# Optimization experiments

Measured on AMD Instinct MI355X. Metric: run time of the kernel, lower is better.

The kernel has to match this reference:

```python
import jax, jax.numpy as jnp
import numpy as np

GRID_MIN = np.array([-40.0, -40.0, -2.0], dtype=np.float32)
VOXEL = 0.8
NZ, NY, NX = 10, 100, 100
NVOX = NZ * NY * NX


def setup_inputs() -> dict:
    key = jax.random.key(0)
    ks = jax.random.split(key, 7)
    B, T, V, H, W = 1, 2, 6, 32, 88
    Cg, Co = 48, 256
    lo = jnp.asarray(GRID_MIN)
    hi = jnp.array([40.0, 40.0, 6.0], dtype=jnp.float32)
    u = jax.random.uniform(ks[0], (B, T, V, H, W, 3), dtype=jnp.float32)
    centers = lo + u * (hi - lo)
    gs_features = jax.random.normal(ks[1], (B, T, V, H, W, Cg), dtype=jnp.float32)
    occ_volume = jax.random.normal(ks[2], (B, T, Co, NZ, NY, NX), dtype=jnp.float32)
    W_g2o = jax.random.normal(ks[3], (Cg, Co), dtype=jnp.float32) * 0.1
    b_g2o = jnp.zeros((Co,), dtype=jnp.float32)
    W_o2g = jax.random.normal(ks[4], (Co, Cg), dtype=jnp.float32) * 0.1
    b_o2g = jnp.zeros((Cg,), dtype=jnp.float32)
    return {"centers": centers, "gs_features": gs_features, "occ_volume": occ_volume,
            "W_g2o": W_g2o, "b_g2o": b_g2o, "W_o2g": W_o2g, "b_o2g": b_o2g}


def _scatter_mean(pts, vals):
    # pts: [BT, N, 3], vals: [BT, N, C] -> dense [BT, NVOX, C] voxel means
    BT, N, C = vals.shape
    mins = jnp.asarray(GRID_MIN, dtype=pts.dtype)
    ijk = jnp.floor((pts - mins) / VOXEL).astype(jnp.int32)
    ix, iy, iz = ijk[..., 0], ijk[..., 1], ijk[..., 2]
    valid = (ix >= 0) & (ix < NX) & (iy >= 0) & (iy < NY) & (iz >= 0) & (iz < NZ)
    lin = (jnp.clip(iz, 0, NZ - 1) * (NY * NX)
           + jnp.clip(iy, 0, NY - 1) * NX
           + jnp.clip(ix, 0, NX - 1))
    seg = (jnp.arange(BT, dtype=jnp.int32)[:, None] * NVOX + lin).reshape(-1)
    m = valid.reshape(-1, 1).astype(vals.dtype)
    vsum = jax.ops.segment_sum(vals.reshape(-1, C) * m, seg, num_segments=BT * NVOX)
    cnt = jax.ops.segment_sum(m, seg, num_segments=BT * NVOX)
    return (vsum / jnp.maximum(cnt, 1.0)).reshape(BT, NVOX, C)


def _trilinear_sample(occ_sp, pts):
    # occ_sp: [BT, NVOX, C] (z-major), pts: [BT, N, 3] metric xyz
    # grid_sample semantics: align_corners=False, padding_mode='zeros'
    mins = jnp.asarray(GRID_MIN, dtype=pts.dtype)
    dims = jnp.array([NX * VOXEL, NY * VOXEL, NZ * VOXEL], dtype=pts.dtype)
    g = (pts - mins) / jnp.maximum(dims, 1e-6) * 2.0 - 1.0  # normalized xyz in [-1,1]
    sizes = jnp.array([NX, NY, NZ], dtype=pts.dtype)
    pix = ((g + 1.0) * sizes - 1.0) * 0.5  # unnormalized pixel coords (x,y,z)
    p0 = jnp.floor(pix)
    frac = pix - p0  # fractional part, weight of the +1 corner
    p0i = p0.astype(jnp.int32)
    out = jnp.zeros(occ_sp.shape[:1] + pts.shape[1:2] + occ_sp.shape[-1:], occ_sp.dtype)
    bounds = (NX, NY, NZ)
    for dz in (0, 1):
        for dy in (0, 1):
            for dx in (0, 1):
                d = (dx, dy, dz)
                idxs = [p0i[..., a] + d[a] for a in range(3)]
                inb = ((idxs[0] >= 0) & (idxs[0] < NX)
                       & (idxs[1] >= 0) & (idxs[1] < NY)
                       & (idxs[2] >= 0) & (idxs[2] < NZ))
                w = jnp.ones_like(frac[..., 0])
                for a in range(3):
                    w = w * jnp.where(d[a] == 1, frac[..., a], 1.0 - frac[..., a])
                lin = (jnp.clip(idxs[2], 0, NZ - 1) * (NY * NX)
                       + jnp.clip(idxs[1], 0, NY - 1) * NX
                       + jnp.clip(idxs[0], 0, NX - 1))
                corner = jnp.take_along_axis(occ_sp, lin[..., None], axis=1)
                out = out + corner * (w * inb.astype(w.dtype))[..., None]
    return out  # [BT, N, C]


def reference(centers, gs_features, occ_volume, W_g2o, b_g2o, W_o2g, b_o2g):
    B, T, V, H, W, _ = centers.shape
    BT, N = B * T, V * H * W
    Co = occ_volume.shape[2]
    pts = centers.reshape(BT, N, 3)
    feats = gs_features.reshape(BT, N, gs_features.shape[-1])
    # gs -> occ: linear proj then voxel scatter-mean
    vals = feats @ W_g2o + b_g2o  # [BT, N, Co]
    vol = _scatter_mean(pts, vals)  # [BT, NVOX, Co]
    gs_to_occ = vol.reshape(B, T, NZ, NY, NX, Co).transpose(0, 1, 5, 2, 3, 4)
    # occ -> gs: trilinear sample then linear proj
    occ_sp = occ_volume.reshape(BT, Co, NVOX).transpose(0, 2, 1)  # [BT, NVOX, Co]
    sampled = _trilinear_sample(occ_sp, pts)  # [BT, N, Co]
    occ_to_gs = (sampled @ W_o2g + b_o2g).reshape(B, T, V, H, W, -1)
    return gs_to_occ, occ_to_gs
```

## Files before the change

kernel.cpp:

```cpp
#include <hip/hip_runtime.h>
#include <hip/hip_bf16.h>

typedef float v4f __attribute__((ext_vector_type(4)));
typedef short v4s __attribute__((ext_vector_type(4)));
typedef short bfrag8 __attribute__((ext_vector_type(8)));

constexpr int NXc = 100, NYc = 100, NZc = 10;
constexpr int NVOX = NZc * NYc * NXc;
constexpr int CO = 256, CG = 48;
constexpr int BT = 2;
constexpr int NPT = 6 * 32 * 88;
constexpr int NPTS = BT * NPT;
constexpr int MAXS = NPTS;
constexpr int NW64 = (NVOX + 63) / 64;
constexpr int NB_VP = (BT * NW64 + 3) / 4;
constexpr int NB_SC = NPTS * CG / 256;
constexpr int NB_WV = (NVOX + 1023) / 1024;
constexpr int NB_WR = NB_WV * 8 * BT;
constexpr int NB_GA = NPTS * CG / 256;
constexpr float GMX = -40.0f, GMY = -40.0f, GMZ = -2.0f;
constexpr float VOXEL = 0.8f;

static __device__ __forceinline__ short f2bf(float f) {
    __hip_bfloat16 h = __float2bfloat16(f);
    return __builtin_bit_cast(short, h);
}
static __device__ __forceinline__ float bf2f(unsigned short u) {
    unsigned v = (unsigned)u << 16;
    return __builtin_bit_cast(float, v);
}

__global__ __launch_bounds__(256) void k_init(
    v4f* __restrict__ p, int n16,
    const float* __restrict__ Wo2g, short* __restrict__ wp)
{
    if (blockIdx.x < 1024) {
        v4f z = {0.f, 0.f, 0.f, 0.f};
        for (int i = blockIdx.x * 256 + threadIdx.x; i < n16; i += 1024 * 256)
            p[i] = z;
    } else {
        for (int e = threadIdx.x; e < 8 * 3 * 64 * 8; e += 256) {
            int j  = e & 7;
            int l  = (e >> 3) & 63;
            int ft = e >> 9;
            int s  = ft / 3, gt = ft - 3 * s;
            int k  = s * 32 + (l >> 4) * 8 + j;
            int g  = gt * 16 + (l & 15);
            wp[e] = f2bf(Wo2g[k * CG + g]);
        }
    }
}

__global__ __launch_bounds__(256) void k_count(
    const float* __restrict__ pts, float* __restrict__ cnt,
    int* __restrict__ nocc, int* __restrict__ invmap, int* __restrict__ ptvox,
    int* __restrict__ list)
{
    int pn = blockIdx.x * 256 + threadIdx.x;
    float x = pts[pn * 3 + 0];
    float y = pts[pn * 3 + 1];
    float z = pts[pn * 3 + 2];
    int ix = (int)floorf((x - GMX) / VOXEL);
    int iy = (int)floorf((y - GMY) / VOXEL);
    int iz = (int)floorf((z - GMZ) / VOXEL);
    bool valid = (ix >= 0 && ix < NXc && iy >= 0 && iy < NYc && iz >= 0 && iz < NZc);
    if (!valid) { ptvox[pn] = -1; return; }
    int bt = pn / NPT;
    int btvox = bt * NVOX + iz * (NYc * NXc) + iy * NXc + ix;
    ptvox[pn] = btvox;
    float old = atomicAdd(&cnt[btvox], 1.0f);
    if (old == 0.0f) {
        int s = atomicAdd(nocc, 1);
        invmap[btvox] = s + 1;
        list[s] = btvox;
    }
}

__global__ __launch_bounds__(256) void k_megaA(
    const float* __restrict__ occ, const short* __restrict__ wp,
    unsigned short* __restrict__ P,
    const float* __restrict__ feats, const int* __restrict__ ptvox,
    const int* __restrict__ invmap, float* __restrict__ compactM)
{
    int bid = blockIdx.x;
    int vpq = bid / 9;
    bool is_vp = (bid % 9 == 0) && (vpq < NB_VP);
    if (is_vp) {
        int gwid = (vpq * 256 + threadIdx.x) >> 6;
        if (gwid >= BT * NW64) return;
        int l = threadIdx.x & 63;
        int q = l >> 4, r = l & 15;
        const bfrag8* wf = reinterpret_cast<const bfrag8*>(wp);
        bfrag8 wfr[8][3];
#pragma unroll
        for (int s = 0; s < 8; ++s)
#pragma unroll
            for (int gt = 0; gt < 3; ++gt)
                wfr[s][gt] = wf[(s * 3 + gt) * 64 + l];
        int bt = gwid / NW64;
        int vox0 = (gwid - bt * NW64) * 64;
        int vbase = vox0 + 4 * r;
        int vload = vbase > NVOX - 4 ? NVOX - 4 : vbase;
        const float* b0 = occ + (size_t)bt * CO * NVOX + (size_t)q * 8 * NVOX + vload;
        v4f acc[4][3];
#pragma unroll
        for (int t = 0; t < 4; ++t)
#pragma unroll
            for (int gt = 0; gt < 3; ++gt)
                acc[t][gt] = v4f{0.f, 0.f, 0.f, 0.f};
#pragma unroll
        for (int s = 0; s < 8; ++s) {
            v4f vj[8];
#pragma unroll
            for (int j = 0; j < 8; ++j)
                vj[j] = *reinterpret_cast<const v4f*>(b0 + (size_t)(s * 32 + j) * NVOX);
            bfrag8 bf[4];
#pragma unroll
            for (int t = 0; t < 4; ++t)
#pragma unroll
                for (int j = 0; j < 8; ++j)
                    bf[t][j] = f2bf(vj[j][t]);
#pragma unroll
            for (int t = 0; t < 4; ++t)
#pragma unroll
                for (int gt = 0; gt < 3; ++gt)
                    acc[t][gt] = __builtin_amdgcn_mfma_f32_16x16x32_bf16(
                        wfr[s][gt], bf[t], acc[t][gt], 0, 0, 0);
        }
        unsigned short* o = P + ((size_t)bt * NVOX + vbase) * CG + q * 4;
#pragma unroll
        for (int t = 0; t < 4; ++t) {
            if (vbase + t < NVOX) {
#pragma unroll
                for (int gt = 0; gt < 3; ++gt) {
                    v4s pk;
#pragma unroll
                    for (int e = 0; e < 4; ++e) pk[e] = f2bf(acc[t][gt][e]);
                    *reinterpret_cast<v4s*>(o + t * CG + gt * 16) = pk;
                }
            }
        }
    } else {
        int nvp = (bid + 8) / 9; if (nvp > NB_VP) nvp = NB_VP;
        int scid = bid - nvp;
        int idx = scid * 256 + threadIdx.x;
        int k  = idx % CG;
        int pn = idx / CG;
        int bv = ptvox[pn];
        if (bv < 0) return;
        int slot = invmap[bv] - 1;
        atomicAdd(&compactM[(size_t)slot * CG + k], feats[idx]);
    }
}

__global__ __launch_bounds__(256) void k_gemm(
    const float* __restrict__ compactM, const float* __restrict__ cnt,
    const int* __restrict__ list, const int* __restrict__ noccp,
    const float* __restrict__ Wg2o, const float* __restrict__ bg2o,
    float* __restrict__ compact256)
{
    int nocc = *noccp;
    int s0 = blockIdx.x * 32;
    if (s0 >= nocc) return;
    __shared__ float Wl[CG * CO];
    __shared__ float Ml[32 * CG];
    for (int j = threadIdx.x; j < CG * CO; j += 256) Wl[j] = Wg2o[j];
    for (int j = threadIdx.x; j < 32 * CG; j += 256) {
        int v = j / CG, k = j - v * CG;
        int slot = s0 + v;
        float m = 0.f;
        if (slot < nocc) {
            int btvox = list[slot];
            m = compactM[(size_t)slot * CG + k] / cnt[btvox];
        }
        Ml[j] = m;
    }
    __syncthreads();
    int wid = threadIdx.x >> 6, l = threadIdx.x & 63;
    int vb = wid * 8;
    float4 bias = *reinterpret_cast<const float4*>(&bg2o[4 * l]);
    float acc[8][4];
#pragma unroll
    for (int v = 0; v < 8; ++v) {
        acc[v][0] = bias.x; acc[v][1] = bias.y; acc[v][2] = bias.z; acc[v][3] = bias.w;
    }
    for (int k = 0; k < CG; k += 4) {
        float4 w0 = *reinterpret_cast<const float4*>(&Wl[(k + 0) * CO + 4 * l]);
        float4 w1 = *reinterpret_cast<const float4*>(&Wl[(k + 1) * CO + 4 * l]);
        float4 w2 = *reinterpret_cast<const float4*>(&Wl[(k + 2) * CO + 4 * l]);
        float4 w3 = *reinterpret_cast<const float4*>(&Wl[(k + 3) * CO + 4 * l]);
#pragma unroll
        for (int v = 0; v < 8; ++v) {
            float4 m4 = *reinterpret_cast<const float4*>(&Ml[(vb + v) * CG + k]);
            acc[v][0] = fmaf(m4.x, w0.x, acc[v][0]);
            acc[v][1] = fmaf(m4.x, w0.y, acc[v][1]);
            acc[v][2] = fmaf(m4.x, w0.z, acc[v][2]);
            acc[v][3] = fmaf(m4.x, w0.w, acc[v][3]);
            acc[v][0] = fmaf(m4.y, w1.x, acc[v][0]);
            acc[v][1] = fmaf(m4.y, w1.y, acc[v][1]);
            acc[v][2] = fmaf(m4.y, w1.z, acc[v][2]);
            acc[v][3] = fmaf(m4.y, w1.w, acc[v][3]);
            acc[v][0] = fmaf(m4.z, w2.x, acc[v][0]);
            acc[v][1] = fmaf(m4.z, w2.y, acc[v][1]);
            acc[v][2] = fmaf(m4.z, w2.z, acc[v][2]);
            acc[v][3] = fmaf(m4.z, w2.w, acc[v][3]);
            acc[v][0] = fmaf(m4.w, w3.x, acc[v][0]);
            acc[v][1] = fmaf(m4.w, w3.y, acc[v][1]);
            acc[v][2] = fmaf(m4.w, w3.z, acc[v][2]);
            acc[v][3] = fmaf(m4.w, w3.w, acc[v][3]);
        }
    }
#pragma unroll
    for (int v = 0; v < 8; ++v) {
        int slot = s0 + vb + v;
        if (slot < nocc) {
            float4 rr; rr.x = acc[v][0]; rr.y = acc[v][1]; rr.z = acc[v][2]; rr.w = acc[v][3];
            *reinterpret_cast<float4*>(&compact256[(size_t)slot * CO + 4 * l]) = rr;
        }
    }
}

__global__ __launch_bounds__(256) void k_megaB(
    const int* __restrict__ invmap, const float* __restrict__ compact256,
    float* __restrict__ out0,
    const float* __restrict__ pts, const unsigned short* __restrict__ P,
    const float* __restrict__ bo2g, float* __restrict__ out1)
{
    __shared__ float ldsT[32][260];
    int bid = blockIdx.x;
    int wrq = bid / 5;
    bool is_wr = (bid % 5 == 0) && (wrq < NB_WR);
    if (is_wr) {
        int bt  = wrq / (NB_WV * 8);
        int rem = wrq - bt * (NB_WV * 8);
        int c0  = (rem / NB_WV) * 32;
        int vb  = (rem - (rem / NB_WV) * NB_WV) * 1024;
        int tid = threadIdx.x;
        int w = tid >> 6, l = tid & 63;
        float* ob = out0 + (size_t)bt * CO * NVOX;
#pragma unroll
        for (int sc = 0; sc < 4; ++sc) {
            int vbase = vb + sc * 256;
            int vox = vbase + tid;
            int slot = (vox < NVOX) ? invmap[bt * NVOX + vox] : 0;
            if (slot > 0) {
                const v4f* row = reinterpret_cast<const v4f*>(
                    compact256 + (size_t)(slot - 1) * CO + c0);
#pragma unroll
                for (int cq = 0; cq < 8; ++cq) {
                    v4f d = row[cq];
#pragma unroll
                    for (int i = 0; i < 4; ++i) ldsT[cq * 4 + i][tid] = d[i];
                }
            } else {
#pragma unroll
                for (int c = 0; c < 32; ++c) ldsT[c][tid] = 0.f;
            }
            __syncthreads();
#pragma unroll
            for (int u = 0; u < 8; ++u) {
                int ci = u * 4 + w;
                int vq = 4 * l;
                int vv = vbase + vq;
                if (vv < NVOX) {
                    v4f val = *reinterpret_cast<const v4f*>(&ldsT[ci][vq]);
                    __builtin_nontemporal_store(val,
                        reinterpret_cast<v4f*>(ob + (size_t)(c0 + ci) * NVOX + vv));
                }
            }
            if (sc < 3) __syncthreads();
        }
    } else {
        int nwr = (bid + 4) / 5; if (nwr > NB_WR) nwr = NB_WR;
        int gaid = bid - nwr;
        int idx = gaid * 256 + threadIdx.x;
        int g  = idx % CG;
        int pn = idx / CG;
        int bt = pn / NPT;
        float x = pts[pn * 3 + 0];
        float y = pts[pn * 3 + 1];
        float z = pts[pn * 3 + 2];
        float gx = (x - GMX) / 80.0f * 2.0f - 1.0f;
        float gy = (y - GMY) / 80.0f * 2.0f - 1.0f;
        float gz = (z - GMZ) / 8.0f  * 2.0f - 1.0f;
        float px = ((gx + 1.0f) * (float)NXc - 1.0f) * 0.5f;
        float py = ((gy + 1.0f) * (float)NYc - 1.0f) * 0.5f;
        float pz = ((gz + 1.0f) * (float)NZc - 1.0f) * 0.5f;
        float fx = floorf(px), fy = floorf(py), fz = floorf(pz);
        float rx = px - fx, ry = py - fy, rz = pz - fz;
        int x0 = (int)fx, y0 = (int)fy, z0 = (int)fz;
        float acc = bo2g[g];
        const unsigned short* Pb = P + (size_t)bt * NVOX * CG;
#pragma unroll
        for (int dz = 0; dz <= 1; ++dz) {
            int zi = z0 + dz;
            if (zi < 0 || zi >= NZc) continue;
            float wz = dz ? rz : 1.0f - rz;
#pragma unroll
            for (int dy = 0; dy <= 1; ++dy) {
                int yi = y0 + dy;
                if (yi < 0 || yi >= NYc) continue;
                float wy = dy ? ry : 1.0f - ry;
#pragma unroll
                for (int dx = 0; dx <= 1; ++dx) {
                    int xi = x0 + dx;
                    if (xi < 0 || xi >= NXc) continue;
                    float wx = dx ? rx : 1.0f - rx;
                    float w = (wx * wy) * wz;
                    int lin = zi * (NYc * NXc) + yi * NXc + xi;
                    acc = fmaf(w, bf2f(Pb[(size_t)lin * CG + g]), acc);
                }
            }
        }
        out1[idx] = acc;
    }
}

extern "C" void kernel_launch(void* const* d_in, const int* in_sizes, int n_in,
                              void* d_out, int out_size, void* d_ws, size_t ws_size,
                              hipStream_t stream)
{
    const float* centers = (const float*)d_in[0];
    const float* feats   = (const float*)d_in[1];
    const float* occ     = (const float*)d_in[2];
    const float* Wg2o    = (const float*)d_in[3];
    const float* bg2o    = (const float*)d_in[4];
    const float* Wo2g    = (const float*)d_in[5];
    const float* bo2g    = (const float*)d_in[6];

    float* out  = (float*)d_out;
    float* out0 = out;
    float* out1 = out + (size_t)BT * CO * NVOX;
    short* wp   = (short*)out1;

    char* w = (char*)d_ws;
    float* cnt       = (float*)w;                 w += (size_t)BT * NVOX * 4;
    int*   nocc      = (int*)w;                   w += 256;
    int*   invmap    = (int*)w;                   w += (size_t)BT * NVOX * 4;
    float* compactM  = (float*)w;                 w += (size_t)MAXS * CG * 4;
    size_t zbytes = (size_t)BT * NVOX * 4 + 256 + (size_t)BT * NVOX * 4
                  + (size_t)MAXS * CG * 4;
    int*   ptvox     = (int*)w;                   w += (size_t)NPTS * 4;
    int*   list      = (int*)w;                   w += (size_t)MAXS * 4;
    float* compact256= (float*)w;                 w += (size_t)MAXS * CO * 4;
    unsigned short* P = (unsigned short*)w;

    k_init<<<1025, 256, 0, stream>>>((v4f*)d_ws, (int)(zbytes / 16), Wo2g, wp);
    k_count<<<NPTS / 256, 256, 0, stream>>>(centers, cnt, nocc, invmap, ptvox, list);
    k_megaA<<<NB_VP + NB_SC, 256, 0, stream>>>(occ, wp, P, feats, ptvox, invmap, compactM);
    k_gemm<<<(MAXS + 31) / 32, 256, 0, stream>>>(compactM, cnt, list, nocc, Wg2o, bg2o, compact256);
    k_megaB<<<NB_WR + NB_GA, 256, 0, stream>>>(invmap, compact256, out0, centers, P, bo2g, out1);
}
```

Before: 144.9 us.

## Store compact voxel means as bf16 and stream weight fragments in megaA

The compacted per-voxel 256-channel projection buffer is now written in bf16 by the gemm kernel and converted back to float when megaB transposes it into the dense output. This halves intermediate traffic for the gather-transpose stage. megaA also stops preloading all 24 weight fragments into registers, loading each per step instead, and adds a launch-bounds occupancy hint to cut register pressure. The cost is bf16 rounding in the gs_to_occ output and extra weight reloads.

```diff
diff --git a/kernel.cpp b/kernel.cpp
--- a/kernel.cpp
+++ b/kernel.cpp
@@ -3,6 +3,7 @@
 
 typedef float v4f __attribute__((ext_vector_type(4)));
 typedef short v4s __attribute__((ext_vector_type(4)));
+typedef short v8s __attribute__((ext_vector_type(8)));
 typedef short bfrag8 __attribute__((ext_vector_type(8)));
 
 constexpr int NXc = 100, NYc = 100, NZc = 10;
@@ -76,7 +77,7 @@
     }
 }
 
-__global__ __launch_bounds__(256) void k_megaA(
+__global__ __launch_bounds__(256, 4) void k_megaA(
     const float* __restrict__ occ, const short* __restrict__ wp,
     unsigned short* __restrict__ P,
     const float* __restrict__ feats, const int* __restrict__ ptvox,
@@ -91,12 +92,6 @@
         int l = threadIdx.x & 63;
         int q = l >> 4, r = l & 15;
         const bfrag8* wf = reinterpret_cast<const bfrag8*>(wp);
-        bfrag8 wfr[8][3];
-#pragma unroll
-        for (int s = 0; s < 8; ++s)
-#pragma unroll
-            for (int gt = 0; gt < 3; ++gt)
-                wfr[s][gt] = wf[(s * 3 + gt) * 64 + l];
         int bt = gwid / NW64;
         int vox0 = (gwid - bt * NW64) * 64;
         int vbase = vox0 + 4 * r;
@@ -121,11 +116,13 @@
                 for (int j = 0; j < 8; ++j)
                     bf[t][j] = f2bf(vj[j][t]);
 #pragma unroll
-            for (int t = 0; t < 4; ++t)
-#pragma unroll
-                for (int gt = 0; gt < 3; ++gt)
+            for (int gt = 0; gt < 3; ++gt) {
+                bfrag8 a = wf[(s * 3 + gt) * 64 + l];
+#pragma unroll
+                for (int t = 0; t < 4; ++t)
                     acc[t][gt] = __builtin_amdgcn_mfma_f32_16x16x32_bf16(
-                        wfr[s][gt], bf[t], acc[t][gt], 0, 0, 0);
+                        a, bf[t], acc[t][gt], 0, 0, 0);
+            }
         }
         unsigned short* o = P + ((size_t)bt * NVOX + vbase) * CG + q * 4;
 #pragma unroll
@@ -157,7 +154,7 @@
     const float* __restrict__ compactM, const float* __restrict__ cnt,
     const int* __restrict__ list, const int* __restrict__ noccp,
     const float* __restrict__ Wg2o, const float* __restrict__ bg2o,
-    float* __restrict__ compact256)
+    unsigned short* __restrict__ compact256h)
 {
     int nocc = *noccp;
     int s0 = blockIdx.x * 32;
@@ -214,14 +211,16 @@
     for (int v = 0; v < 8; ++v) {
         int slot = s0 + vb + v;
         if (slot < nocc) {
-            float4 rr; rr.x = acc[v][0]; rr.y = acc[v][1]; rr.z = acc[v][2]; rr.w = acc[v][3];
-            *reinterpret_cast<float4*>(&compact256[(size_t)slot * CO + 4 * l]) = rr;
+            v4s rr;
+#pragma unroll
+            for (int e = 0; e < 4; ++e) rr[e] = f2bf(acc[v][e]);
+            *reinterpret_cast<v4s*>(&compact256h[(size_t)slot * CO + 4 * l]) = rr;
         }
     }
 }
 
 __global__ __launch_bounds__(256) void k_megaB(
-    const int* __restrict__ invmap, const float* __restrict__ compact256,
+    const int* __restrict__ invmap, const unsigned short* __restrict__ compact256h,
     float* __restrict__ out0,
     const float* __restrict__ pts, const unsigned short* __restrict__ P,
     const float* __restrict__ bo2g, float* __restrict__ out1)
@@ -244,13 +243,14 @@
             int vox = vbase + tid;
             int slot = (vox < NVOX) ? invmap[bt * NVOX + vox] : 0;
             if (slot > 0) {
-                const v4f* row = reinterpret_cast<const v4f*>(
-                    compact256 + (size_t)(slot - 1) * CO + c0);
-#pragma unroll
-                for (int cq = 0; cq < 8; ++cq) {
-                    v4f d = row[cq];
-#pragma unroll
-                    for (int i = 0; i < 4; ++i) ldsT[cq * 4 + i][tid] = d[i];
+                const v8s* row = reinterpret_cast<const v8s*>(
+                    compact256h + (size_t)(slot - 1) * CO + c0);
+#pragma unroll
+                for (int cq = 0; cq < 4; ++cq) {
+                    v8s d = row[cq];
+#pragma unroll
+                    for (int i = 0; i < 8; ++i)
+                        ldsT[cq * 8 + i][tid] = bf2f((unsigned short)d[i]);
                 }
             } else {
 #pragma unroll
@@ -342,12 +342,12 @@
                   + (size_t)MAXS * CG * 4;
     int*   ptvox     = (int*)w;                   w += (size_t)NPTS * 4;
     int*   list      = (int*)w;                   w += (size_t)MAXS * 4;
-    float* compact256= (float*)w;                 w += (size_t)MAXS * CO * 4;
+    unsigned short* compact256h = (unsigned short*)w;  w += (size_t)MAXS * CO * 2;
     unsigned short* P = (unsigned short*)w;
 
     k_init<<<1025, 256, 0, stream>>>((v4f*)d_ws, (int)(zbytes / 16), Wo2g, wp);
     k_count<<<NPTS / 256, 256, 0, stream>>>(centers, cnt, nocc, invmap, ptvox, list);
     k_megaA<<<NB_VP + NB_SC, 256, 0, stream>>>(occ, wp, P, feats, ptvox, invmap, compactM);
-    k_gemm<<<(MAXS + 31) / 32, 256, 0, stream>>>(compactM, cnt, list, nocc, Wg2o, bg2o, compact256);
-    k_megaB<<<NB_WR + NB_GA, 256, 0, stream>>>(invmap, compact256, out0, centers, P, bo2g, out1);
-}
+    k_gemm<<<(MAXS + 31) / 32, 256, 0, stream>>>(compactM, cnt, list, nocc, Wg2o, bg2o, compact256h);
+    k_megaB<<<NB_WR + NB_GA, 256, 0, stream>>>(invmap, compact256h, out0, centers, P, bo2g, out1);
+}
```

New measurement: 142.3 us. About the same (-1.8%).
